# Kernel tuning notes

Hardware: AMD Instinct MI355X
Metric: run time of the kernel (lower is better)

Reference implementation:

```python
import jax, jax.numpy as jnp
import numpy as np

GROUP_SIZE = 128
TOP_K = 2
ZERO_POINT = 8  # Marlin symmetric zero point: w = scale * (q - 8)


def _dequant_int4(q, scales, group_size):
    # q: [E, N, K] int values in [0,15]; scales: [E, N, K//group_size]
    s = jnp.repeat(scales, group_size, axis=-1)  # [E, N, K]
    return (q.astype(jnp.float32) - float(ZERO_POINT)) * s


def setup_inputs() -> dict:
    key = jax.random.key(0)
    k1, k2, k3, k4, k5, k6 = jax.random.split(key, 6)
    B, S, H, I, E = 2, 1024, 2048, 1408, 8
    router_logits = jax.random.normal(k1, (B, S, E), dtype=jnp.float32)
    hidden_states = jax.random.normal(k2, (B, S, H), dtype=jnp.float32)
    fc_gate_up_qweights = jax.random.randint(k3, (E, 2 * I, H), 0, 16, dtype=jnp.int32)
    fc_gate_up_scales = jax.random.uniform(k4, (E, 2 * I, H // GROUP_SIZE), dtype=jnp.float32) * 0.02
    fc_down_qweights = jax.random.randint(k5, (E, H, I), 0, 16, dtype=jnp.int32)
    fc_down_scales = jax.random.uniform(k6, (E, H, I // GROUP_SIZE), dtype=jnp.float32) * 0.02
    return {
        "router_logits": router_logits,
        "hidden_states": hidden_states,
        "fc_gate_up_qweights": fc_gate_up_qweights,
        "fc_gate_up_scales": fc_gate_up_scales,
        "fc_down_qweights": fc_down_qweights,
        "fc_down_scales": fc_down_scales,
    }


def reference(router_logits, hidden_states, fc_gate_up_qweights, fc_gate_up_scales,
              fc_down_qweights, fc_down_scales):
    B, S, H = hidden_states.shape
    E = router_logits.shape[-1]
    T = B * S
    x = hidden_states.reshape(T, H)
    logits = router_logits.reshape(T, E)

    # top-k routing with softmax over selected logits
    top_vals, top_idx = jax.lax.top_k(logits, TOP_K)          # [T, k]
    top_w = jax.nn.softmax(top_vals, axis=-1)                 # [T, k]
    route_w = jnp.zeros((T, E), x.dtype).at[jnp.arange(T)[:, None], top_idx].set(top_w)  # [T, E]

    # dequantize int4 weights: scale * (q - 8), per-group along K
    w_gate_up = _dequant_int4(fc_gate_up_qweights, fc_gate_up_scales, GROUP_SIZE)  # [E, 2I, H]
    w_down = _dequant_int4(fc_down_qweights, fc_down_scales, GROUP_SIZE)          # [E, H, I]

    # grouped GEMM (dense over experts, masked by routing weights)
    gu = jnp.einsum('th,enh->ten', x, w_gate_up)              # [T, E, 2I]
    gate, up = jnp.split(gu, 2, axis=-1)
    act = jax.nn.silu(gate) * up                              # SwiGLU, [T, E, I]
    out = jnp.einsum('tei,ehi,te->th', act, w_down, route_w)  # [T, H]
    return out.reshape(B, S, H)
```

## Files before the change

kernel.cpp:

```cpp
#include <hip/hip_runtime.h>
#include <hip/hip_bf16.h>

#define T_TOKENS 2048
#define H_DIM    2048
#define I_DIM    1408
#define E_NUM    8

typedef __bf16 bf16;
typedef __attribute__((ext_vector_type(8))) __bf16  bf16x8;
typedef __attribute__((ext_vector_type(4))) float   floatx4;

static const size_t OFF_COUNTS = 0;
static const size_t OFF_LISTS  = 256;
static const size_t OFF_WLISTS = OFF_LISTS + (size_t)T_TOKENS * E_NUM * 4;
static const size_t OFF_XB     = 131328;
static const size_t OFF_ACT    = OFF_XB + (size_t)T_TOKENS * H_DIM * 2;
static const size_t OFF_GUPK   = OFF_ACT + (size_t)2 * T_TOKENS * I_DIM * 2;
static const size_t OFF_DNPK   = OFF_GUPK + (size_t)E_NUM * 22 * 32 * 16384;
static const size_t OFF_TMP    = OFF_GUPK;

__global__ __launch_bounds__(256) void pack_gu_kernel(const int* __restrict__ q,
                                                      const float* __restrict__ sc,
                                                      bf16* __restrict__ out)
{
    const int b = blockIdx.x;
    const int t = threadIdx.x;
    const int e = b / 2816;
    const int grow = b - e * 2816;
    const int4* qp = reinterpret_cast<const int4*>(q + (size_t)b * H_DIM) + t * 2;
    int4 a = qp[0], c = qp[1];
    float s = sc[(size_t)b * 16 + (t >> 4)];
    float m8s = -8.f * s;
    bf16x8 bv;
    bv[0] = (bf16)fmaf((float)a.x, s, m8s);
    bv[1] = (bf16)fmaf((float)a.y, s, m8s);
    bv[2] = (bf16)fmaf((float)a.z, s, m8s);
    bv[3] = (bf16)fmaf((float)a.w, s, m8s);
    bv[4] = (bf16)fmaf((float)c.x, s, m8s);
    bv[5] = (bf16)fmaf((float)c.y, s, m8s);
    bv[6] = (bf16)fmaf((float)c.z, s, m8s);
    bv[7] = (bf16)fmaf((float)c.w, s, m8s);
    const int is_up = grow >= I_DIM;
    const int icol  = grow - (is_up ? I_DIM : 0);
    const int nt    = icol >> 6;
    const int r     = ((((icol >> 4) & 3) * 2 + is_up) * 16) + (icol & 15);
    size_t dst = ((((size_t)e * 22 + nt) * 32 + (t >> 3)) * 128 + r) * 8 + ((t & 7) ^ (r & 7));
    reinterpret_cast<bf16x8*>(out)[dst] = bv;
}

__global__ __launch_bounds__(256) void pack_dn_kernel(const int* __restrict__ q,
                                                      const float* __restrict__ sc,
                                                      bf16* __restrict__ out)
{
    const int b = blockIdx.x;
    const int t = threadIdx.x;
    if (t >= 176) return;
    const int e = b >> 11;
    const int grow = b & 2047;
    const int4* qp = reinterpret_cast<const int4*>(q + (size_t)b * I_DIM) + t * 2;
    int4 a = qp[0], c = qp[1];
    float s = sc[(size_t)b * 11 + (t >> 4)];
    float m8s = -8.f * s;
    bf16x8 bv;
    bv[0] = (bf16)fmaf((float)a.x, s, m8s);
    bv[1] = (bf16)fmaf((float)a.y, s, m8s);
    bv[2] = (bf16)fmaf((float)a.z, s, m8s);
    bv[3] = (bf16)fmaf((float)a.w, s, m8s);
    bv[4] = (bf16)fmaf((float)c.x, s, m8s);
    bv[5] = (bf16)fmaf((float)c.y, s, m8s);
    bv[6] = (bf16)fmaf((float)c.z, s, m8s);
    bv[7] = (bf16)fmaf((float)c.w, s, m8s);
    const int nt = grow >> 7;
    const int r  = grow & 127;
    size_t dst = ((((size_t)e * 16 + nt) * 22 + (t >> 3)) * 128 + r) * 8 + ((t & 7) ^ (r & 7));
    reinterpret_cast<bf16x8*>(out)[dst] = bv;
}

__global__ void xconv_kernel(const float* __restrict__ x, bf16* __restrict__ xb)
{
    int i = blockIdx.x * blockDim.x + threadIdx.x;
    const float4* x4 = reinterpret_cast<const float4*>(x) + (size_t)i * 2;
    float4 v0 = x4[0], v1 = x4[1];
    bf16x8 bv;
    bv[0] = (bf16)v0.x; bv[1] = (bf16)v0.y; bv[2] = (bf16)v0.z; bv[3] = (bf16)v0.w;
    bv[4] = (bf16)v1.x; bv[5] = (bf16)v1.y; bv[6] = (bf16)v1.z; bv[7] = (bf16)v1.w;
    *reinterpret_cast<bf16x8*>(xb + (size_t)i * 8) = bv;
}

__global__ void router_kernel(const float* __restrict__ logits,
                              int* __restrict__ counts,
                              int* __restrict__ lists,
                              float* __restrict__ wlists)
{
    int t = blockIdx.x * blockDim.x + threadIdx.x;
    if (t >= T_TOKENS) return;
    const float* l = logits + (size_t)t * E_NUM;
    float v0 = -1e30f, v1 = -1e30f;
    int i0 = 0, i1 = 0;
    #pragma unroll
    for (int e = 0; e < E_NUM; ++e) {
        float v = l[e];
        if (v > v0) { v1 = v0; i1 = i0; v0 = v; i0 = e; }
        else if (v > v1) { v1 = v; i1 = e; }
    }
    float w0 = 1.f / (1.f + __expf(v1 - v0));
    float w1 = 1.f - w0;
    int p0 = atomicAdd(&counts[i0], 1);
    lists[i0 * T_TOKENS + p0] = t * 2 + 0;
    wlists[i0 * T_TOKENS + p0] = w0;
    int p1 = atomicAdd(&counts[i1], 1);
    lists[i1 * T_TOKENS + p1] = t * 2 + 1;
    wlists[i1 * T_TOKENS + p1] = w1;
}

__global__ __launch_bounds__(256) void gemm1_kernel(
    const bf16* __restrict__ xb,
    const bf16* __restrict__ wpk,
    const int*  __restrict__ counts,
    const int*  __restrict__ lists,
    bf16*       __restrict__ act)
{
    const int e   = blockIdx.z;
    const int cnt = counts[e];
    const int m0  = blockIdx.y * 128;
    if (m0 >= cnt) return;
    const int nt  = blockIdx.x;

    __shared__ __align__(16) bf16 Al[8192];
    __shared__ __align__(16) bf16 Bl[8192];
    __shared__ int meta[128];

    const int tid = threadIdx.x;
    if (tid < 128) {
        int m = m0 + tid;
        meta[tid] = lists[e * T_TOKENS + (m < cnt ? m : 0)];
    }
    __syncthreads();

    const int lane = tid & 63;
    const int wv = tid >> 6;
    const int wm = wv >> 1, wn = wv & 1;

    int    aoff[4];
    size_t agbl[4];
    #pragma unroll
    for (int j = 0; j < 4; ++j) {
        int g = tid + 256 * j;
        int arow = g >> 3, cg = g & 7;
        aoff[j] = arow * 64 + ((cg ^ (arow & 7)) * 8);
        agbl[j] = (size_t)(meta[arow] >> 1) * H_DIM + cg * 8;
    }
    const bf16* bt = wpk + ((size_t)e * 22 + nt) * (32 * 8192) + tid * 8;

    int afr[2][4], bfr[2][4];
    #pragma unroll
    for (int ks = 0; ks < 2; ++ks) {
        int gidx = ks * 4 + (lane >> 4);
        #pragma unroll
        for (int t4 = 0; t4 < 4; ++t4) {
            int ra = wm * 64 + t4 * 16 + (lane & 15);
            afr[ks][t4] = ra * 64 + ((gidx ^ (ra & 7)) * 8);
            int rb = wn * 64 + t4 * 16 + (lane & 15);
            bfr[ks][t4] = rb * 64 + ((gidx ^ (rb & 7)) * 8);
        }
    }

    floatx4 acc[4][4];
    #pragma unroll
    for (int i = 0; i < 4; ++i)
        #pragma unroll
        for (int j = 0; j < 4; ++j)
            acc[i][j] = (floatx4){0.f, 0.f, 0.f, 0.f};

    for (int k0 = 0; k0 < H_DIM; k0 += 64) {
        #pragma unroll
        for (int j = 0; j < 4; ++j) {
            bf16x8 v = *reinterpret_cast<const bf16x8*>(xb + agbl[j] + k0);
            *reinterpret_cast<bf16x8*>(&Al[aoff[j]]) = v;
        }
        const bf16* bsrc = bt + (size_t)(k0 >> 6) * 8192;
        #pragma unroll
        for (int j = 0; j < 4; ++j) {
            bf16x8 v = *reinterpret_cast<const bf16x8*>(bsrc + j * 2048);
            *reinterpret_cast<bf16x8*>(&Bl[tid * 8 + j * 2048]) = v;
        }
        __syncthreads();
        #pragma unroll
        for (int ks = 0; ks < 2; ++ks) {
            bf16x8 af[4], bff[4];
            #pragma unroll
            for (int mt = 0; mt < 4; ++mt)
                af[mt] = *reinterpret_cast<const bf16x8*>(&Al[afr[ks][mt]]);
            #pragma unroll
            for (int ntf = 0; ntf < 4; ++ntf)
                bff[ntf] = *reinterpret_cast<const bf16x8*>(&Bl[bfr[ks][ntf]]);
            #pragma unroll
            for (int mt = 0; mt < 4; ++mt)
                #pragma unroll
                for (int ntf = 0; ntf < 4; ++ntf)
                    acc[mt][ntf] = __builtin_amdgcn_mfma_f32_16x16x32_bf16(af[mt], bff[ntf], acc[mt][ntf], 0, 0, 0);
        }
        __syncthreads();
    }

    const int rbase = (lane >> 4) * 4;
    const int cn = lane & 15;
    #pragma unroll
    for (int mt = 0; mt < 4; ++mt) {
        #pragma unroll
        for (int j = 0; j < 2; ++j) {
            floatx4 g = acc[mt][2 * j];
            floatx4 u = acc[mt][2 * j + 1];
            int col = nt * 64 + (wn * 2 + j) * 16 + cn;
            #pragma unroll
            for (int r = 0; r < 4; ++r) {
                int lrow = wm * 64 + mt * 16 + rbase + r;
                if (m0 + lrow < cnt) {
                    float gate = g[r], up = u[r];
                    float a = gate / (1.f + __expf(-gate)) * up;
                    act[(size_t)meta[lrow] * I_DIM + col] = (bf16)a;
                }
            }
        }
    }
}

__global__ __launch_bounds__(256) void gemm2_kernel(
    const bf16*  __restrict__ act,
    const bf16*  __restrict__ wpk,
    const int*   __restrict__ counts,
    const int*   __restrict__ lists,
    const float* __restrict__ wlists,
    float*       __restrict__ tmp)
{
    const int e   = blockIdx.z;
    const int cnt = counts[e];
    const int m0  = blockIdx.y * 128;
    if (m0 >= cnt) return;
    const int nt  = blockIdx.x;

    __shared__ __align__(16) bf16 Al[8192];
    __shared__ __align__(16) bf16 Bl[8192];
    __shared__ int   meta[128];
    __shared__ float wmeta[128];

    const int tid = threadIdx.x;
    if (tid < 128) {
        int m = m0 + tid;
        int mm = (m < cnt) ? m : 0;
        meta[tid]  = lists[e * T_TOKENS + mm];
        wmeta[tid] = wlists[e * T_TOKENS + mm];
    }
    __syncthreads();

    const int lane = tid & 63;
    const int wv = tid >> 6;
    const int wm = wv >> 1, wn = wv & 1;

    int    aoff[4];
    size_t agbl[4];
    #pragma unroll
    for (int j = 0; j < 4; ++j) {
        int g = tid + 256 * j;
        int arow = g >> 3, cg = g & 7;
        aoff[j] = arow * 64 + ((cg ^ (arow & 7)) * 8);
        agbl[j] = (size_t)meta[arow] * I_DIM + cg * 8;
    }
    const bf16* bt = wpk + ((size_t)e * 16 + nt) * (22 * 8192) + tid * 8;

    int afr[2][4], bfr[2][4];
    #pragma unroll
    for (int ks = 0; ks < 2; ++ks) {
        int gidx = ks * 4 + (lane >> 4);
        #pragma unroll
        for (int t4 = 0; t4 < 4; ++t4) {
            int ra = wm * 64 + t4 * 16 + (lane & 15);
            afr[ks][t4] = ra * 64 + ((gidx ^ (ra & 7)) * 8);
            int rb = wn * 64 + t4 * 16 + (lane & 15);
            bfr[ks][t4] = rb * 64 + ((gidx ^ (rb & 7)) * 8);
        }
    }

    floatx4 acc[4][4];
    #pragma unroll
    for (int i = 0; i < 4; ++i)
        #pragma unroll
        for (int j = 0; j < 4; ++j)
            acc[i][j] = (floatx4){0.f, 0.f, 0.f, 0.f};

    for (int kt = 0; kt < 22; ++kt) {
        #pragma unroll
        for (int j = 0; j < 4; ++j) {
            bf16x8 v = *reinterpret_cast<const bf16x8*>(act + agbl[j] + kt * 64);
            *reinterpret_cast<bf16x8*>(&Al[aoff[j]]) = v;
        }
        const bf16* bsrc = bt + (size_t)kt * 8192;
        #pragma unroll
        for (int j = 0; j < 4; ++j) {
            bf16x8 v = *reinterpret_cast<const bf16x8*>(bsrc + j * 2048);
            *reinterpret_cast<bf16x8*>(&Bl[tid * 8 + j * 2048]) = v;
        }
        __syncthreads();
        #pragma unroll
        for (int ks = 0; ks < 2; ++ks) {
            bf16x8 af[4], bff[4];
            #pragma unroll
            for (int mt = 0; mt < 4; ++mt)
                af[mt] = *reinterpret_cast<const bf16x8*>(&Al[afr[ks][mt]]);
            #pragma unroll
            for (int ntf = 0; ntf < 4; ++ntf)
                bff[ntf] = *reinterpret_cast<const bf16x8*>(&Bl[bfr[ks][ntf]]);
            #pragma unroll
            for (int mt = 0; mt < 4; ++mt)
                #pragma unroll
                for (int ntf = 0; ntf < 4; ++ntf)
                    acc[mt][ntf] = __builtin_amdgcn_mfma_f32_16x16x32_bf16(af[mt], bff[ntf], acc[mt][ntf], 0, 0, 0);
        }
        __syncthreads();
    }

    const int rbase = (lane >> 4) * 4;
    const int cn = lane & 15;
    #pragma unroll
    for (int mt = 0; mt < 4; ++mt) {
        #pragma unroll
        for (int ntf = 0; ntf < 4; ++ntf) {
            floatx4 v = acc[mt][ntf];
            int col = nt * 128 + wn * 64 + ntf * 16 + cn;
            #pragma unroll
            for (int r = 0; r < 4; ++r) {
                int lrow = wm * 64 + mt * 16 + rbase + r;
                if (m0 + lrow < cnt) {
                    tmp[(size_t)meta[lrow] * H_DIM + col] = wmeta[lrow] * v[r];
                }
            }
        }
    }
}

__global__ void finalize_kernel(const float* __restrict__ tmp, float* __restrict__ out)
{
    int i4 = blockIdx.x * blockDim.x + threadIdx.x;
    int t  = i4 >> 9;
    int h  = (i4 & 511) * 4;
    float4 a = *reinterpret_cast<const float4*>(tmp + ((size_t)2 * t) * H_DIM + h);
    float4 b = *reinterpret_cast<const float4*>(tmp + ((size_t)(2 * t + 1)) * H_DIM + h);
    float4 o;
    o.x = a.x + b.x; o.y = a.y + b.y; o.z = a.z + b.z; o.w = a.w + b.w;
    *reinterpret_cast<float4*>(out + (size_t)t * H_DIM + h) = o;
}

extern "C" void kernel_launch(void* const* d_in, const int* in_sizes, int n_in,
                              void* d_out, int out_size, void* d_ws, size_t ws_size,
                              hipStream_t stream)
{
    const float* router_logits = (const float*)d_in[0];
    const float* x             = (const float*)d_in[1];
    const int*   gu_q          = (const int*)d_in[2];
    const float* gu_s          = (const float*)d_in[3];
    const int*   dn_q          = (const int*)d_in[4];
    const float* dn_s          = (const float*)d_in[5];
    float* out = (float*)d_out;

    char* ws = (char*)d_ws;
    int*   counts = (int*)(ws + OFF_COUNTS);
    int*   lists  = (int*)(ws + OFF_LISTS);
    float* wlists = (float*)(ws + OFF_WLISTS);
    bf16*  xb     = (bf16*)(ws + OFF_XB);
    bf16*  act    = (bf16*)(ws + OFF_ACT);
    bf16*  gu_pk  = (bf16*)(ws + OFF_GUPK);
    bf16*  dn_pk  = (bf16*)(ws + OFF_DNPK);
    float* tmp    = (float*)(ws + OFF_TMP);

    hipMemsetAsync(counts, 0, E_NUM * sizeof(int), stream);

    pack_gu_kernel<<<E_NUM * 2816, 256, 0, stream>>>(gu_q, gu_s, gu_pk);
    pack_dn_kernel<<<E_NUM * 2048, 256, 0, stream>>>(dn_q, dn_s, dn_pk);
    xconv_kernel<<<T_TOKENS * H_DIM / 8 / 256, 256, 0, stream>>>(x, xb);
    router_kernel<<<T_TOKENS / 256, 256, 0, stream>>>(router_logits, counts, lists, wlists);

    gemm1_kernel<<<dim3(22, 16, 8), 256, 0, stream>>>(xb, gu_pk, counts, lists, act);
    gemm2_kernel<<<dim3(16, 16, 8), 256, 0, stream>>>(act, dn_pk, counts, lists, wlists, tmp);
    finalize_kernel<<<4096, 256, 0, stream>>>(tmp, out);
}
```

Before: 522.2 us.

## Keep weights packed as int4 and dequantize to fp16 inside GEMM tiles

The pack kernels now store nibble-packed int4 weights, four bits per value, instead of dequantized bf16 values. This cuts the pack-kernel write traffic and the GEMM weight reads by roughly four times. The GEMMs load the scales into shared memory and dequantize in registers with the 0x6400 fp16 magic-number trick, then run f16 MFMA. Activations switch from bf16 to fp16. The cost is extra ALU work in the inner loop, plus a risk of fp16 range or precision problems on the activations and on the scale products.

```diff
diff --git a/kernel.cpp b/kernel.cpp
--- a/kernel.cpp
+++ b/kernel.cpp
@@ -1,14 +1,15 @@
 #include <hip/hip_runtime.h>
-#include <hip/hip_bf16.h>
+#include <hip/hip_fp16.h>
 
 #define T_TOKENS 2048
 #define H_DIM    2048
 #define I_DIM    1408
 #define E_NUM    8
 
-typedef __bf16 bf16;
-typedef __attribute__((ext_vector_type(8))) __bf16  bf16x8;
-typedef __attribute__((ext_vector_type(4))) float   floatx4;
+typedef _Float16 f16;
+typedef __attribute__((ext_vector_type(8))) _Float16 f16x8;
+typedef __attribute__((ext_vector_type(4))) float    floatx4;
+typedef __attribute__((ext_vector_type(4))) unsigned uintx4;
 
 static const size_t OFF_COUNTS = 0;
 static const size_t OFF_LISTS  = 256;
@@ -16,75 +17,60 @@
 static const size_t OFF_XB     = 131328;
 static const size_t OFF_ACT    = OFF_XB + (size_t)T_TOKENS * H_DIM * 2;
 static const size_t OFF_GUPK   = OFF_ACT + (size_t)2 * T_TOKENS * I_DIM * 2;
-static const size_t OFF_DNPK   = OFF_GUPK + (size_t)E_NUM * 22 * 32 * 16384;
-static const size_t OFF_TMP    = OFF_GUPK;
+static const size_t OFF_DNPK   = OFF_GUPK + (size_t)E_NUM * 22 * 32 * 128 * 8 * 4;
+static const size_t OFF_TMP    = OFF_DNPK + (size_t)E_NUM * 16 * 22 * 128 * 8 * 4;
+
 
 __global__ __launch_bounds__(256) void pack_gu_kernel(const int* __restrict__ q,
-                                                      const float* __restrict__ sc,
-                                                      bf16* __restrict__ out)
+                                                      unsigned* __restrict__ out)
 {
     const int b = blockIdx.x;
-    const int t = threadIdx.x;
+    const int g = threadIdx.x;
+    const int4* qp = reinterpret_cast<const int4*>(q + (size_t)b * H_DIM) + g * 2;
+    int4 a = qp[0], c = qp[1];
+    unsigned d = (unsigned)(a.x & 15)        | ((unsigned)(a.z & 15) << 4)  |
+                 ((unsigned)(c.x & 15) << 8) | ((unsigned)(c.z & 15) << 12) |
+                 ((unsigned)(a.y & 15) << 16)| ((unsigned)(a.w & 15) << 20) |
+                 ((unsigned)(c.y & 15) << 24)| ((unsigned)(c.w & 15) << 28);
     const int e = b / 2816;
     const int grow = b - e * 2816;
-    const int4* qp = reinterpret_cast<const int4*>(q + (size_t)b * H_DIM) + t * 2;
-    int4 a = qp[0], c = qp[1];
-    float s = sc[(size_t)b * 16 + (t >> 4)];
-    float m8s = -8.f * s;
-    bf16x8 bv;
-    bv[0] = (bf16)fmaf((float)a.x, s, m8s);
-    bv[1] = (bf16)fmaf((float)a.y, s, m8s);
-    bv[2] = (bf16)fmaf((float)a.z, s, m8s);
-    bv[3] = (bf16)fmaf((float)a.w, s, m8s);
-    bv[4] = (bf16)fmaf((float)c.x, s, m8s);
-    bv[5] = (bf16)fmaf((float)c.y, s, m8s);
-    bv[6] = (bf16)fmaf((float)c.z, s, m8s);
-    bv[7] = (bf16)fmaf((float)c.w, s, m8s);
     const int is_up = grow >= I_DIM;
     const int icol  = grow - (is_up ? I_DIM : 0);
     const int nt    = icol >> 6;
     const int r     = ((((icol >> 4) & 3) * 2 + is_up) * 16) + (icol & 15);
-    size_t dst = ((((size_t)e * 22 + nt) * 32 + (t >> 3)) * 128 + r) * 8 + ((t & 7) ^ (r & 7));
-    reinterpret_cast<bf16x8*>(out)[dst] = bv;
+    const int kt    = g >> 3, gg = g & 7;
+    out[((((size_t)e * 22 + nt) * 32 + kt) * 128 + r) * 8 + (gg ^ (r & 7))] = d;
 }
 
 __global__ __launch_bounds__(256) void pack_dn_kernel(const int* __restrict__ q,
-                                                      const float* __restrict__ sc,
-                                                      bf16* __restrict__ out)
+                                                      unsigned* __restrict__ out)
 {
     const int b = blockIdx.x;
     const int t = threadIdx.x;
     if (t >= 176) return;
+    const int4* qp = reinterpret_cast<const int4*>(q + (size_t)b * I_DIM) + t * 2;
+    int4 a = qp[0], c = qp[1];
+    unsigned d = (unsigned)(a.x & 15)        | ((unsigned)(a.z & 15) << 4)  |
+                 ((unsigned)(c.x & 15) << 8) | ((unsigned)(c.z & 15) << 12) |
+                 ((unsigned)(a.y & 15) << 16)| ((unsigned)(a.w & 15) << 20) |
+                 ((unsigned)(c.y & 15) << 24)| ((unsigned)(c.w & 15) << 28);
     const int e = b >> 11;
     const int grow = b & 2047;
-    const int4* qp = reinterpret_cast<const int4*>(q + (size_t)b * I_DIM) + t * 2;
-    int4 a = qp[0], c = qp[1];
-    float s = sc[(size_t)b * 11 + (t >> 4)];
-    float m8s = -8.f * s;
-    bf16x8 bv;
-    bv[0] = (bf16)fmaf((float)a.x, s, m8s);
-    bv[1] = (bf16)fmaf((float)a.y, s, m8s);
-    bv[2] = (bf16)fmaf((float)a.z, s, m8s);
-    bv[3] = (bf16)fmaf((float)a.w, s, m8s);
-    bv[4] = (bf16)fmaf((float)c.x, s, m8s);
-    bv[5] = (bf16)fmaf((float)c.y, s, m8s);
-    bv[6] = (bf16)fmaf((float)c.z, s, m8s);
-    bv[7] = (bf16)fmaf((float)c.w, s, m8s);
     const int nt = grow >> 7;
     const int r  = grow & 127;
-    size_t dst = ((((size_t)e * 16 + nt) * 22 + (t >> 3)) * 128 + r) * 8 + ((t & 7) ^ (r & 7));
-    reinterpret_cast<bf16x8*>(out)[dst] = bv;
-}
-
-__global__ void xconv_kernel(const float* __restrict__ x, bf16* __restrict__ xb)
+    const int kt = t >> 3, gg = t & 7;
+    out[((((size_t)e * 16 + nt) * 22 + kt) * 128 + r) * 8 + (gg ^ (r & 7))] = d;
+}
+
+__global__ void xconv_kernel(const float* __restrict__ x, f16* __restrict__ xb)
 {
     int i = blockIdx.x * blockDim.x + threadIdx.x;
     const float4* x4 = reinterpret_cast<const float4*>(x) + (size_t)i * 2;
     float4 v0 = x4[0], v1 = x4[1];
-    bf16x8 bv;
-    bv[0] = (bf16)v0.x; bv[1] = (bf16)v0.y; bv[2] = (bf16)v0.z; bv[3] = (bf16)v0.w;
-    bv[4] = (bf16)v1.x; bv[5] = (bf16)v1.y; bv[6] = (bf16)v1.z; bv[7] = (bf16)v1.w;
-    *reinterpret_cast<bf16x8*>(xb + (size_t)i * 8) = bv;
+    f16x8 bv;
+    bv[0] = (f16)v0.x; bv[1] = (f16)v0.y; bv[2] = (f16)v0.z; bv[3] = (f16)v0.w;
+    bv[4] = (f16)v1.x; bv[5] = (f16)v1.y; bv[6] = (f16)v1.z; bv[7] = (f16)v1.w;
+    *reinterpret_cast<f16x8*>(xb + (size_t)i * 8) = bv;
 }
 
 __global__ void router_kernel(const float* __restrict__ logits,
@@ -113,12 +99,28 @@
     wlists[i1 * T_TOKENS + p1] = w1;
 }
 
+__device__ __forceinline__ f16x8 dq8(unsigned d, __half2 s2)
+{
+    const __half2 off = __floats2half2_rn(1032.f, 1032.f);
+    unsigned t0 = (d         & 0x000F000Fu) | 0x64006400u;
+    unsigned t1 = ((d >> 4)  & 0x000F000Fu) | 0x64006400u;
+    unsigned t2 = ((d >> 8)  & 0x000F000Fu) | 0x64006400u;
+    unsigned t3 = ((d >> 12) & 0x000F000Fu) | 0x64006400u;
+    uintx4 w;
+    w.x = __builtin_bit_cast(unsigned, __hmul2(__hsub2(__builtin_bit_cast(__half2, t0), off), s2));
+    w.y = __builtin_bit_cast(unsigned, __hmul2(__hsub2(__builtin_bit_cast(__half2, t1), off), s2));
+    w.z = __builtin_bit_cast(unsigned, __hmul2(__hsub2(__builtin_bit_cast(__half2, t2), off), s2));
+    w.w = __builtin_bit_cast(unsigned, __hmul2(__hsub2(__builtin_bit_cast(__half2, t3), off), s2));
+    return __builtin_bit_cast(f16x8, w);
+}
+
 __global__ __launch_bounds__(256) void gemm1_kernel(
-    const bf16* __restrict__ xb,
-    const bf16* __restrict__ wpk,
-    const int*  __restrict__ counts,
-    const int*  __restrict__ lists,
-    bf16*       __restrict__ act)
+    const f16*      __restrict__ xb,
+    const unsigned* __restrict__ qpk,
+    const float*    __restrict__ sc,
+    const int*      __restrict__ counts,
+    const int*      __restrict__ lists,
+    f16*            __restrict__ act)
 {
     const int e   = blockIdx.z;
     const int cnt = counts[e];
@@ -126,14 +128,21 @@
     if (m0 >= cnt) return;
     const int nt  = blockIdx.x;
 
-    __shared__ __align__(16) bf16 Al[8192];
-    __shared__ __align__(16) bf16 Bl[8192];
+    __shared__ __align__(16) f16 Al[8192];
+    __shared__ unsigned Blu[1024];
+    __shared__ float scl[128 * 17];
     __shared__ int meta[128];
 
     const int tid = threadIdx.x;
     if (tid < 128) {
         int m = m0 + tid;
         meta[tid] = lists[e * T_TOKENS + (m < cnt ? m : 0)];
+    }
+    for (int i = tid; i < 2048; i += 256) {
+        int r = i >> 4, grp = i & 15;
+        int tt = r >> 4, within = r & 15;
+        int grow = ((tt & 1) ? I_DIM : 0) + nt * 64 + (tt >> 1) * 16 + within;
+        scl[r * 17 + grp] = sc[(size_t)(e * 2816 + grow) * 16 + grp];
     }
     __syncthreads();
 
@@ -150,20 +159,7 @@
         aoff[j] = arow * 64 + ((cg ^ (arow & 7)) * 8);
         agbl[j] = (size_t)(meta[arow] >> 1) * H_DIM + cg * 8;
     }
-    const bf16* bt = wpk + ((size_t)e * 22 + nt) * (32 * 8192) + tid * 8;
-
-    int afr[2][4], bfr[2][4];
-    #pragma unroll
-    for (int ks = 0; ks < 2; ++ks) {
-        int gidx = ks * 4 + (lane >> 4);
-        #pragma unroll
-        for (int t4 = 0; t4 < 4; ++t4) {
-            int ra = wm * 64 + t4 * 16 + (lane & 15);
-            afr[ks][t4] = ra * 64 + ((gidx ^ (ra & 7)) * 8);
-            int rb = wn * 64 + t4 * 16 + (lane & 15);
-            bfr[ks][t4] = rb * 64 + ((gidx ^ (rb & 7)) * 8);
-        }
-    }
+    const unsigned* bt = qpk + ((size_t)e * 22 + nt) * (32 * 1024);
 
     floatx4 acc[4][4];
     #pragma unroll
@@ -172,33 +168,40 @@
         for (int j = 0; j < 4; ++j)
             acc[i][j] = (floatx4){0.f, 0.f, 0.f, 0.f};
 
-    for (int k0 = 0; k0 < H_DIM; k0 += 64) {
+    for (int kt = 0; kt < 32; ++kt) {
         #pragma unroll
         for (int j = 0; j < 4; ++j) {
-            bf16x8 v = *reinterpret_cast<const bf16x8*>(xb + agbl[j] + k0);
-            *reinterpret_cast<bf16x8*>(&Al[aoff[j]]) = v;
-        }
-        const bf16* bsrc = bt + (size_t)(k0 >> 6) * 8192;
-        #pragma unroll
-        for (int j = 0; j < 4; ++j) {
-            bf16x8 v = *reinterpret_cast<const bf16x8*>(bsrc + j * 2048);
-            *reinterpret_cast<bf16x8*>(&Bl[tid * 8 + j * 2048]) = v;
-        }
+            f16x8 v = *reinterpret_cast<const f16x8*>(xb + agbl[j] + kt * 64);
+            *reinterpret_cast<f16x8*>(&Al[aoff[j]]) = v;
+        }
+        const unsigned* bsrc = bt + kt * 1024;
+        #pragma unroll
+        for (int j = 0; j < 4; ++j)
+            Blu[tid + j * 256] = bsrc[tid + j * 256];
         __syncthreads();
+
+        const int grp = kt >> 1;
         #pragma unroll
         for (int ks = 0; ks < 2; ++ks) {
-            bf16x8 af[4], bff[4];
-            #pragma unroll
-            for (int mt = 0; mt < 4; ++mt)
-                af[mt] = *reinterpret_cast<const bf16x8*>(&Al[afr[ks][mt]]);
-            #pragma unroll
-            for (int ntf = 0; ntf < 4; ++ntf)
-                bff[ntf] = *reinterpret_cast<const bf16x8*>(&Bl[bfr[ks][ntf]]);
+            const int gidx = ks * 4 + (lane >> 4);
+            f16x8 af[4], bf[4];
+            #pragma unroll
+            for (int mt = 0; mt < 4; ++mt) {
+                int ra = wm * 64 + mt * 16 + (lane & 15);
+                af[mt] = *reinterpret_cast<const f16x8*>(&Al[ra * 64 + ((gidx ^ (ra & 7)) * 8)]);
+            }
+            #pragma unroll
+            for (int ntf = 0; ntf < 4; ++ntf) {
+                int rb = wn * 64 + ntf * 16 + (lane & 15);
+                __half2 s2 = __float2half2_rn(scl[rb * 17 + grp]);
+                unsigned d = Blu[rb * 8 + (gidx ^ (rb & 7))];
+                bf[ntf] = dq8(d, s2);
+            }
             #pragma unroll
             for (int mt = 0; mt < 4; ++mt)
                 #pragma unroll
                 for (int ntf = 0; ntf < 4; ++ntf)
-                    acc[mt][ntf] = __builtin_amdgcn_mfma_f32_16x16x32_bf16(af[mt], bff[ntf], acc[mt][ntf], 0, 0, 0);
+                    acc[mt][ntf] = __builtin_amdgcn_mfma_f32_16x16x32_f16(af[mt], bf[ntf], acc[mt][ntf], 0, 0, 0);
         }
         __syncthreads();
     }
@@ -218,7 +221,7 @@
                 if (m0 + lrow < cnt) {
                     float gate = g[r], up = u[r];
                     float a = gate / (1.f + __expf(-gate)) * up;
-                    act[(size_t)meta[lrow] * I_DIM + col] = (bf16)a;
+                    act[(size_t)meta[lrow] * I_DIM + col] = (f16)a;
                 }
             }
         }
@@ -226,12 +229,13 @@
 }
 
 __global__ __launch_bounds__(256) void gemm2_kernel(
-    const bf16*  __restrict__ act,
-    const bf16*  __restrict__ wpk,
-    const int*   __restrict__ counts,
-    const int*   __restrict__ lists,
-    const float* __restrict__ wlists,
-    float*       __restrict__ tmp)
+    const f16*      __restrict__ act,
+    const unsigned* __restrict__ qpk,
+    const float*    __restrict__ sc,
+    const int*      __restrict__ counts,
+    const int*      __restrict__ lists,
+    const float*    __restrict__ wlists,
+    float*          __restrict__ tmp)
 {
     const int e   = blockIdx.z;
     const int cnt = counts[e];
@@ -239,8 +243,9 @@
     if (m0 >= cnt) return;
     const int nt  = blockIdx.x;
 
-    __shared__ __align__(16) bf16 Al[8192];
-    __shared__ __align__(16) bf16 Bl[8192];
+    __shared__ __align__(16) f16 Al[8192];
+    __shared__ unsigned Blu[1024];
+    __shared__ float scl[128 * 12];
     __shared__ int   meta[128];
     __shared__ float wmeta[128];
 
@@ -251,6 +256,10 @@
         meta[tid]  = lists[e * T_TOKENS + mm];
         wmeta[tid] = wlists[e * T_TOKENS + mm];
     }
+    for (int i = tid; i < 1408; i += 256) {
+        int r = i / 11, grp = i - r * 11;
+        scl[r * 12 + grp] = sc[(size_t)(e * 2048 + nt * 128 + r) * 11 + grp];
+    }
     __syncthreads();
 
     const int lane = tid & 63;
@@ -266,20 +275,7 @@
         aoff[j] = arow * 64 + ((cg ^ (arow & 7)) * 8);
         agbl[j] = (size_t)meta[arow] * I_DIM + cg * 8;
     }
-    const bf16* bt = wpk + ((size_t)e * 16 + nt) * (22 * 8192) + tid * 8;
-
-    int afr[2][4], bfr[2][4];
-    #pragma unroll
-    for (int ks = 0; ks < 2; ++ks) {
-        int gidx = ks * 4 + (lane >> 4);
-        #pragma unroll
-        for (int t4 = 0; t4 < 4; ++t4) {
-            int ra = wm * 64 + t4 * 16 + (lane & 15);
-            afr[ks][t4] = ra * 64 + ((gidx ^ (ra & 7)) * 8);
-            int rb = wn * 64 + t4 * 16 + (lane & 15);
-            bfr[ks][t4] = rb * 64 + ((gidx ^ (rb & 7)) * 8);
-        }
-    }
+    const unsigned* bt = qpk + ((size_t)e * 16 + nt) * (22 * 1024);
 
     floatx4 acc[4][4];
     #pragma unroll
@@ -291,30 +287,37 @@
     for (int kt = 0; kt < 22; ++kt) {
         #pragma unroll
         for (int j = 0; j < 4; ++j) {
-            bf16x8 v = *reinterpret_cast<const bf16x8*>(act + agbl[j] + kt * 64);
-            *reinterpret_cast<bf16x8*>(&Al[aoff[j]]) = v;
-        }
-        const bf16* bsrc = bt + (size_t)kt * 8192;
-        #pragma unroll
-        for (int j = 0; j < 4; ++j) {
-            bf16x8 v = *reinterpret_cast<const bf16x8*>(bsrc + j * 2048);
-            *reinterpret_cast<bf16x8*>(&Bl[tid * 8 + j * 2048]) = v;
-        }
+            f16x8 v = *reinterpret_cast<const f16x8*>(act + agbl[j] + kt * 64);
+            *reinterpret_cast<f16x8*>(&Al[aoff[j]]) = v;
+        }
+        const unsigned* bsrc = bt + kt * 1024;
+        #pragma unroll
+        for (int j = 0; j < 4; ++j)
+            Blu[tid + j * 256] = bsrc[tid + j * 256];
         __syncthreads();
+
+        const int grp = kt >> 1;
         #pragma unroll
         for (int ks = 0; ks < 2; ++ks) {
-            bf16x8 af[4], bff[4];
-            #pragma unroll
-            for (int mt = 0; mt < 4; ++mt)
-                af[mt] = *reinterpret_cast<const bf16x8*>(&Al[afr[ks][mt]]);
-            #pragma unroll
-            for (int ntf = 0; ntf < 4; ++ntf)
-                bff[ntf] = *reinterpret_cast<const bf16x8*>(&Bl[bfr[ks][ntf]]);
+            const int gidx = ks * 4 + (lane >> 4);
+            f16x8 af[4], bf[4];
+            #pragma unroll
+            for (int mt = 0; mt < 4; ++mt) {
+                int ra = wm * 64 + mt * 16 + (lane & 15);
+                af[mt] = *reinterpret_cast<const f16x8*>(&Al[ra * 64 + ((gidx ^ (ra & 7)) * 8)]);
+            }
+            #pragma unroll
+            for (int ntf = 0; ntf < 4; ++ntf) {
+                int rb = wn * 64 + ntf * 16 + (lane & 15);
+                __half2 s2 = __float2half2_rn(scl[rb * 12 + grp]);
+                unsigned d = Blu[rb * 8 + (gidx ^ (rb & 7))];
+                bf[ntf] = dq8(d, s2);
+            }
             #pragma unroll
             for (int mt = 0; mt < 4; ++mt)
                 #pragma unroll
                 for (int ntf = 0; ntf < 4; ++ntf)
-                    acc[mt][ntf] = __builtin_amdgcn_mfma_f32_16x16x32_bf16(af[mt], bff[ntf], acc[mt][ntf], 0, 0, 0);
+                    acc[mt][ntf] = __builtin_amdgcn_mfma_f32_16x16x32_f16(af[mt], bf[ntf], acc[mt][ntf], 0, 0, 0);
         }
         __syncthreads();
     }
@@ -363,23 +366,23 @@
     float* out = (float*)d_out;
 
     char* ws = (char*)d_ws;
-    int*   counts = (int*)(ws + OFF_COUNTS);
-    int*   lists  = (int*)(ws + OFF_LISTS);
-    float* wlists = (float*)(ws + OFF_WLISTS);
-    bf16*  xb     = (bf16*)(ws + OFF_XB);
-    bf16*  act    = (bf16*)(ws + OFF_ACT);
-    bf16*  gu_pk  = (bf16*)(ws + OFF_GUPK);
-    bf16*  dn_pk  = (bf16*)(ws + OFF_DNPK);
-    float* tmp    = (float*)(ws + OFF_TMP);
+    int*      counts = (int*)(ws + OFF_COUNTS);
+    int*      lists  = (int*)(ws + OFF_LISTS);
+    float*    wlists = (float*)(ws + OFF_WLISTS);
+    f16*      xb     = (f16*)(ws + OFF_XB);
+    f16*      act    = (f16*)(ws + OFF_ACT);
+    unsigned* gu_pk  = (unsigned*)(ws + OFF_GUPK);
+    unsigned* dn_pk  = (unsigned*)(ws + OFF_DNPK);
+    float*    tmp    = (float*)(ws + OFF_TMP);
 
     hipMemsetAsync(counts, 0, E_NUM * sizeof(int), stream);
 
-    pack_gu_kernel<<<E_NUM * 2816, 256, 0, stream>>>(gu_q, gu_s, gu_pk);
-    pack_dn_kernel<<<E_NUM * 2048, 256, 0, stream>>>(dn_q, dn_s, dn_pk);
+    pack_gu_kernel<<<E_NUM * 2816, 256, 0, stream>>>(gu_q, gu_pk);
+    pack_dn_kernel<<<E_NUM * 2048, 256, 0, stream>>>(dn_q, dn_pk);
     xconv_kernel<<<T_TOKENS * H_DIM / 8 / 256, 256, 0, stream>>>(x, xb);
     router_kernel<<<T_TOKENS / 256, 256, 0, stream>>>(router_logits, counts, lists, wlists);
 
-    gemm1_kernel<<<dim3(22, 16, 8), 256, 0, stream>>>(xb, gu_pk, counts, lists, act);
-    gemm2_kernel<<<dim3(16, 16, 8), 256, 0, stream>>>(act, dn_pk, counts, lists, wlists, tmp);
+    gemm1_kernel<<<dim3(22, 16, 8), 256, 0, stream>>>(xb, gu_pk, gu_s, counts, lists, act);
+    gemm2_kernel<<<dim3(16, 16, 8), 256, 0, stream>>>(act, dn_pk, dn_s, counts, lists, wlists, tmp);
     finalize_kernel<<<4096, 256, 0, stream>>>(tmp, out);
 }
```

New measurement: 561.1 us. 1.07x slower.
